# Kernel optimization log

Hardware: AMD Instinct MI355X
Metric: run time of the kernel (lower is better)

Reference implementation:

```python
import jax, jax.numpy as jnp
import numpy as np

OBS, ACT, HID, MIX, TOPK = 64, 16, 256, 16, 4
EPS = 1e-5

def _ln(x, g, b):
    m = jnp.mean(x, axis=-1, keepdims=True)
    v = jnp.mean(jnp.square(x - m), axis=-1, keepdims=True)
    return (x - m) * jax.lax.rsqrt(v + EPS) * g + b

def setup_inputs() -> dict:
    key = jax.random.key(0)
    ks = jax.random.split(key, 12)
    B = 16384
    D = OBS + ACT            # 80
    F = HID * MIX            # 4096
    s = lambda fan_in: 1.0 / np.sqrt(fan_in)
    return {
        "x": jax.random.normal(ks[0], (B, OBS), jnp.float32),
        "a": jax.random.normal(ks[1], (B, ACT), jnp.float32),
        "W1": jax.random.uniform(ks[2], (F, D), jnp.float32, -s(D), s(D)),
        "b1": jnp.zeros((F,), jnp.float32),
        "W2": jax.random.uniform(ks[3], (F, F), jnp.float32, -s(F), s(F)),
        "b2": jnp.zeros((F,), jnp.float32),
        "W3": jax.random.uniform(ks[4], (1, HID), jnp.float32, -s(HID), s(HID)),
        "b3": jnp.zeros((1,), jnp.float32),
        "g1": jnp.ones((F,), jnp.float32),
        "be1": jnp.zeros((F,), jnp.float32),
        "g2": jnp.ones((F,), jnp.float32),
        "be2": jnp.zeros((F,), jnp.float32),
        "Wg": jax.random.uniform(ks[5], (MIX, D), jnp.float32, -s(D), s(D)),
        "bg": jnp.zeros((MIX,), jnp.float32),
    }

def reference(x, a, W1, b1, W2, b2, W3, b3, g1, be1, g2, be2, Wg, bg):
    B = x.shape[0]
    xa = jnp.concatenate([x, a], axis=1)                      # [B, D]
    gate_scores = jax.nn.softmax(xa @ Wg.T + bg, axis=-1)     # [B, MIX]
    topk_vals, topk_idx = jax.lax.top_k(gate_scores, TOPK)    # [B, K]
    # renormalize top-k weights, scatter into dense score tensor
    topk_vals = topk_vals / jnp.sum(topk_vals, axis=-1, keepdims=True)
    scores = jnp.zeros_like(gate_scores).at[
        jnp.arange(B)[:, None], topk_idx].set(topk_vals)      # [B, MIX]
    h = jax.nn.relu(_ln(xa @ W1.T + b1, g1, be1))             # [B, HID*MIX]
    h = jax.nn.relu(_ln(h @ W2.T + b2, g2, be2))              # [B, HID*MIX]
    h = h.reshape(B, HID, MIX)                                # row-major, same as torch
    h = jnp.mean(h * scores[:, None, :], axis=-1)             # [B, HID]
    return h @ W3.T + b3                                      # [B, 1]
```

## Files before the change

### kernel.cpp

```cpp
#include <hip/hip_runtime.h>
#include <stdint.h>

#define OBS 64
#define ACTD 16
#define DIN 80
#define MIX 16
#define FF 4096
#define NB 16384
#define CHUNK 4096
#define KP 96
#define LNEPS 1e-5f

typedef float f32x4 __attribute__((ext_vector_type(4)));
typedef short bf16x8 __attribute__((ext_vector_type(8)));

__device__ __forceinline__ unsigned short f2bf(float f) {
    union { float f; uint32_t u; } v; v.f = f;
    uint32_t u = v.u;
    u += 0x7fff + ((u >> 16) & 1);
    return (unsigned short)(u >> 16);
}
__device__ __forceinline__ float bf2f(unsigned short h) {
    union { uint32_t u; float f; } v; v.u = ((uint32_t)h) << 16;
    return v.f;
}

__global__ __launch_bounds__(256) void k_conv(const float* __restrict__ W,
                                              unsigned short* __restrict__ O, int n4) {
    int i = blockIdx.x * 256 + threadIdx.x;
    if (i >= n4) return;
    float4 v = ((const float4*)W)[i];
    ushort4 o;
    o.x = f2bf(v.x); o.y = f2bf(v.y); o.z = f2bf(v.z); o.w = f2bf(v.w);
    ((ushort4*)O)[i] = o;
}

__global__ __launch_bounds__(256) void k_prep_x(const float* __restrict__ x, const float* __restrict__ a,
                                                unsigned short* __restrict__ xab) {
    int row = blockIdx.x * 256 + threadIdx.x;
    const float4* xp = (const float4*)(x + (size_t)row * OBS);
    unsigned short* o = xab + (size_t)row * KP;
#pragma unroll
    for (int i = 0; i < 16; ++i) {
        float4 v = xp[i];
        ushort4 u; u.x = f2bf(v.x); u.y = f2bf(v.y); u.z = f2bf(v.z); u.w = f2bf(v.w);
        ((ushort4*)o)[i] = u;
    }
    const float4* ap = (const float4*)(a + (size_t)row * ACTD);
#pragma unroll
    for (int i = 0; i < 4; ++i) {
        float4 v = ap[i];
        ushort4 u; u.x = f2bf(v.x); u.y = f2bf(v.y); u.z = f2bf(v.z); u.w = f2bf(v.w);
        ((ushort4*)(o + OBS))[i] = u;
    }
    ushort4 t0; t0.x = 0x3F80; t0.y = 0; t0.z = 0; t0.w = 0;
    ushort4 z;  z.x = 0; z.y = 0; z.z = 0; z.w = 0;
    ((ushort4*)(o + 80))[0] = t0;
    ((ushort4*)(o + 84))[0] = z;
    ((ushort4*)(o + 88))[0] = z;
    ((ushort4*)(o + 92))[0] = z;
}

__global__ __launch_bounds__(256) void k_prep_w1(const float* __restrict__ W1, const float* __restrict__ b1,
                                                 unsigned short* __restrict__ W1b) {
    int f = blockIdx.x * 256 + threadIdx.x;
    const float4* wp = (const float4*)(W1 + (size_t)f * DIN);
    unsigned short* o = W1b + (size_t)f * KP;
#pragma unroll
    for (int i = 0; i < 20; ++i) {
        float4 v = wp[i];
        ushort4 u; u.x = f2bf(v.x); u.y = f2bf(v.y); u.z = f2bf(v.z); u.w = f2bf(v.w);
        ((ushort4*)o)[i] = u;
    }
    ushort4 t0; t0.x = f2bf(b1[f]); t0.y = 0; t0.z = 0; t0.w = 0;
    ushort4 z;  z.x = 0; z.y = 0; z.z = 0; z.w = 0;
    ((ushort4*)(o + 80))[0] = t0;
    ((ushort4*)(o + 84))[0] = z;
    ((ushort4*)(o + 88))[0] = z;
    ((ushort4*)(o + 92))[0] = z;
}

__global__ __launch_bounds__(256) void k_gate(const float* __restrict__ x, const float* __restrict__ a,
                                              const float* __restrict__ Wg, const float* __restrict__ bg,
                                              float* __restrict__ scores) {
    __shared__ float wgs[MIX * DIN];
    __shared__ float bgs[MIX];
    int t = threadIdx.x;
    for (int e = t; e < MIX * DIN; e += 256) wgs[e] = Wg[e];
    if (t < MIX) bgs[t] = bg[t];
    __syncthreads();
    int row = blockIdx.x * 256 + t;
    float xa[DIN];
    const float4* xp = (const float4*)(x + (size_t)row * OBS);
#pragma unroll
    for (int i = 0; i < OBS / 4; ++i) {
        float4 v = xp[i];
        xa[i*4] = v.x; xa[i*4+1] = v.y; xa[i*4+2] = v.z; xa[i*4+3] = v.w;
    }
    const float4* ap = (const float4*)(a + (size_t)row * ACTD);
#pragma unroll
    for (int i = 0; i < ACTD / 4; ++i) {
        float4 v = ap[i];
        xa[OBS+i*4] = v.x; xa[OBS+i*4+1] = v.y; xa[OBS+i*4+2] = v.z; xa[OBS+i*4+3] = v.w;
    }
    double p[MIX];
    double mx = -1e300;
#pragma unroll
    for (int m = 0; m < MIX; ++m) {
        double acc = (double)bgs[m];
#pragma unroll
        for (int k = 0; k < DIN; ++k) acc += (double)xa[k] * (double)wgs[m*DIN + k];
        p[m] = acc;
        if (acc > mx) mx = acc;
    }
#pragma unroll
    for (int m = 0; m < MIX; ++m) p[m] = exp(p[m] - mx);
    unsigned used = 0;
    double s4 = 0.0;
#pragma unroll
    for (int j = 0; j < 4; ++j) {
        int best = 0; double bv = -1.0;
#pragma unroll
        for (int m = 0; m < MIX; ++m)
            if (!((used >> m) & 1) && p[m] > bv) { bv = p[m]; best = m; }
        used |= 1u << best;
        s4 += bv;
    }
    float* so = scores + (size_t)row * MIX;
#pragma unroll
    for (int m = 0; m < MIX; ++m)
        so[m] = ((used >> m) & 1) ? (float)(p[m] / s4) : 0.f;
}

__global__ __launch_bounds__(256) void k_gemm1(const unsigned short* __restrict__ A,
                                               const unsigned short* __restrict__ B,
                                               unsigned short* __restrict__ C,
                                               float* __restrict__ pstats) {
    __shared__ alignas(16) unsigned short As[128 * 32];
    __shared__ alignas(16) unsigned short Bs[128 * 32];
    int t = threadIdx.x;
    int pm = blockIdx.x & 31;
    int pn = blockIdx.x >> 5;
    int lane = t & 63, wid = t >> 6, wm = wid >> 1, wn = wid & 1;

    const unsigned short* Ap = A + (size_t)pm * 128 * KP;
    const unsigned short* Bp = B + (size_t)pn * 128 * KP;

    f32x4 acc[4][4] = {};

    for (int k0 = 0; k0 < KP; k0 += 32) {
#pragma unroll
        for (int i = 0; i < 2; ++i) {
            int u = t + i * 256;
            int row = u >> 2, p = u & 3;
            int ls = p ^ ((row >> 1) & 3);
            __builtin_amdgcn_global_load_lds(
                (const __attribute__((address_space(1))) void*)(Ap + (size_t)row * KP + k0 + ls * 8),
                (__attribute__((address_space(3))) void*)(As + u * 8), 16, 0, 0);
            __builtin_amdgcn_global_load_lds(
                (const __attribute__((address_space(1))) void*)(Bp + (size_t)row * KP + k0 + ls * 8),
                (__attribute__((address_space(3))) void*)(Bs + u * 8), 16, 0, 0);
        }
        __syncthreads();
        bf16x8 af[4], bfr[4];
#pragma unroll
        for (int mf = 0; mf < 4; ++mf) {
            int r = wm * 64 + mf * 16 + (lane & 15);
            int p = (lane >> 4) ^ ((r >> 1) & 3);
            af[mf] = *(const bf16x8*)(As + r * 32 + p * 8);
        }
#pragma unroll
        for (int nf = 0; nf < 4; ++nf) {
            int r = wn * 64 + nf * 16 + (lane & 15);
            int p = (lane >> 4) ^ ((r >> 1) & 3);
            bfr[nf] = *(const bf16x8*)(Bs + r * 32 + p * 8);
        }
#pragma unroll
        for (int mf = 0; mf < 4; ++mf)
#pragma unroll
            for (int nf = 0; nf < 4; ++nf)
                acc[mf][nf] = __builtin_amdgcn_mfma_f32_16x16x32_bf16(af[mf], bfr[nf], acc[mf][nf], 0, 0, 0);
        __syncthreads();
    }

    int rowbase = pm * 128 + wm * 64 + (lane >> 4) * 4;
    int colbase = pn * 128 + wn * 64 + (lane & 15);
#pragma unroll
    for (int mf = 0; mf < 4; ++mf) {
#pragma unroll
        for (int rr = 0; rr < 4; ++rr) {
            float ss = 0.f, qq = 0.f;
#pragma unroll
            for (int nf = 0; nf < 4; ++nf) {
                float v = acc[mf][nf][rr];
                ss += v; qq += v * v;
                C[(size_t)(rowbase + mf * 16 + rr) * FF + colbase + nf * 16] = f2bf(v);
            }
#pragma unroll
            for (int mask = 1; mask <= 8; mask <<= 1) {
                ss += __shfl_xor(ss, mask);
                qq += __shfl_xor(qq, mask);
            }
            if ((lane & 15) == 0) {
                int row = rowbase + mf * 16 + rr;
                int j = pn * 2 + wn;
                pstats[((size_t)row * 64 + j) * 2 + 0] = ss;
                pstats[((size_t)row * 64 + j) * 2 + 1] = qq;
            }
        }
    }
}

__global__ __launch_bounds__(256) void k_ln1(unsigned short* __restrict__ h1,
                                             const float* __restrict__ pstats,
                                             const float* __restrict__ g1, const float* __restrict__ be1) {
    __shared__ float st[8][2];
    int t = threadIdx.x;
    int r0 = blockIdx.x * 8;
    if (t < 8) {
        float s = 0.f, q = 0.f;
        const float* pp = pstats + (size_t)(r0 + t) * 128;
#pragma unroll
        for (int j = 0; j < 64; ++j) { s += pp[j * 2]; q += pp[j * 2 + 1]; }
        float mu = s / (float)FF;
        float var = q / (float)FF - mu * mu;
        st[t][0] = mu;
        st[t][1] = rsqrtf(var + LNEPS);
    }
    __syncthreads();
    int c = t * 16;
    float g[16], b[16];
#pragma unroll
    for (int q = 0; q < 4; ++q) {
        float4 gv = *(const float4*)(g1 + c + q * 4);
        float4 bv = *(const float4*)(be1 + c + q * 4);
        g[q*4] = gv.x; g[q*4+1] = gv.y; g[q*4+2] = gv.z; g[q*4+3] = gv.w;
        b[q*4] = bv.x; b[q*4+1] = bv.y; b[q*4+2] = bv.z; b[q*4+3] = bv.w;
    }
    for (int r = 0; r < 8; ++r) {
        float mu = st[r][0], rs = st[r][1];
        unsigned short* hp = h1 + (size_t)(r0 + r) * FF + c;
        uint4 u0 = *(const uint4*)hp;
        uint4 u1 = *(const uint4*)(hp + 8);
        uint32_t uu[8] = {u0.x, u0.y, u0.z, u0.w, u1.x, u1.y, u1.z, u1.w};
        uint32_t oo[8];
#pragma unroll
        for (int q = 0; q < 8; ++q) {
            float v0 = bf2f((unsigned short)(uu[q] & 0xffff));
            float v1 = bf2f((unsigned short)(uu[q] >> 16));
            float o0 = fmaxf((v0 - mu) * rs * g[q*2]   + b[q*2],   0.f);
            float o1 = fmaxf((v1 - mu) * rs * g[q*2+1] + b[q*2+1], 0.f);
            oo[q] = (uint32_t)f2bf(o0) | ((uint32_t)f2bf(o1) << 16);
        }
        uint4 w0; w0.x = oo[0]; w0.y = oo[1]; w0.z = oo[2]; w0.w = oo[3];
        uint4 w1; w1.x = oo[4]; w1.y = oo[5]; w1.z = oo[6]; w1.w = oo[7];
        *(uint4*)hp = w0;
        *(uint4*)(hp + 8) = w1;
    }
}

__global__ __launch_bounds__(512, 1) void k_gemm2(const unsigned short* __restrict__ A,
                                                  const unsigned short* __restrict__ B,
                                                  unsigned short* __restrict__ C) {
    constexpr int K = FF;
    constexpr int NKT = K / 64;
    __shared__ alignas(16) unsigned short As[2][2][8192];
    __shared__ alignas(16) unsigned short Bs[2][2][8192];

    int t = threadIdx.x;
    int lane = t & 63, wid = t >> 6;
    int wm = wid >> 2, wn = wid & 3;

    int bid = blockIdx.x;
    int xcd = bid & 7, w = bid >> 3;
    int pm = (xcd >> 1) * 4 + (w >> 3);
    int pn = (xcd & 1) * 8 + (w & 7);

    const unsigned short* Ap = A + (size_t)pm * 256 * K;
    const unsigned short* Bp = B + (size_t)pn * 256 * K;

    f32x4 acc[8][4] = {};
    bf16x8 af[4][2], bfr[4][2];

#define STAGE_H(bq, kt, H)                                                                 \
    {                                                                                      \
        const unsigned short* gsrc = ((H) < 2) ? Ap : Bp;                                  \
        unsigned short* ldst = ((H) < 2) ? &As[(bq)][(H) & 1][0] : &Bs[(bq)][(H) & 1][0];  \
        _Pragma("unroll")                                                                  \
        for (int i = 0; i < 2; ++i) {                                                      \
            int u = i * 512 + t;                                                           \
            int r = u >> 3, sl = u & 7;                                                    \
            __builtin_amdgcn_global_load_lds(                                              \
                (const __attribute__((address_space(1))) void*)(gsrc +                     \
                    (size_t)(((H) & 1) * 128 + r) * K + (kt) * 64 + ((sl ^ (r & 7)) * 8)), \
                (__attribute__((address_space(3))) void*)(ldst + u * 8), 16, 0, 0);        \
        }                                                                                  \
    }

#define RD_AF(bq, mh)                                                           \
    _Pragma("unroll") for (int m = 0; m < 4; ++m) {                             \
        int rr = (mh) * 64 + m * 16 + (lane & 15);                              \
        _Pragma("unroll") for (int kk = 0; kk < 2; ++kk) {                      \
            int sl = (kk * 4 + (lane >> 4)) ^ (rr & 7);                         \
            af[m][kk] = *(const bf16x8*)(&As[(bq)][wm][0] + rr * 64 + sl * 8);  \
        }                                                                       \
    }

#define RD_BF(bq, np)                                                           \
    _Pragma("unroll") for (int n = 0; n < 2; ++n) {                             \
        int cc = wn * 64 + ((np) * 2 + n) * 16 + (lane & 15);                   \
        int hb = cc >> 7, rr = cc & 127;                                        \
        _Pragma("unroll") for (int kk = 0; kk < 2; ++kk) {                      \
            int sl = (kk * 4 + (lane >> 4)) ^ (rr & 7);                         \
            bfr[(np) * 2 + n][kk] = *(const bf16x8*)(&Bs[(bq)][hb][0] + rr * 64 + sl * 8); \
        }                                                                       \
    }

#define MFMA_Q(mh, np)                                                          \
    __builtin_amdgcn_s_barrier();                                               \
    asm volatile("s_waitcnt lgkmcnt(0)" ::: "memory");                          \
    __builtin_amdgcn_sched_barrier(0);                                          \
    __builtin_amdgcn_s_setprio(1);                                              \
    _Pragma("unroll") for (int kk = 0; kk < 2; ++kk)                            \
    _Pragma("unroll") for (int m = 0; m < 4; ++m)                               \
    _Pragma("unroll") for (int n = 0; n < 2; ++n)                               \
        acc[(mh) * 4 + m][(np) * 2 + n] = __builtin_amdgcn_mfma_f32_16x16x32_bf16( \
            af[m][kk], bfr[(np) * 2 + n][kk], acc[(mh) * 4 + m][(np) * 2 + n], 0, 0, 0); \
    __builtin_amdgcn_s_setprio(0);                                              \
    __builtin_amdgcn_sched_barrier(0);

    STAGE_H(0, 0, 0); STAGE_H(0, 0, 1); STAGE_H(0, 0, 2); STAGE_H(0, 0, 3);
    STAGE_H(1, 1, 2); STAGE_H(1, 1, 3);
    asm volatile("s_waitcnt vmcnt(4)" ::: "memory");
    __builtin_amdgcn_s_barrier();

    for (int i = 0; i < NKT / 2; ++i) {
        int tA = 2 * i + 1;
        int tB = 2 * i + 2; if (tB > NKT - 1) tB = NKT - 1;
        int tC = 2 * i + 3; if (tC > NKT - 1) tC = NKT - 1;

        RD_AF(0, 0); RD_BF(0, 0);
        STAGE_H(1, tA, 0);
        MFMA_Q(0, 0);
        __builtin_amdgcn_s_barrier();
        RD_BF(0, 1);
        STAGE_H(1, tA, 1);
        MFMA_Q(0, 1);
        __builtin_amdgcn_s_barrier();
        RD_AF(0, 1);
        STAGE_H(0, tB, 2);
        MFMA_Q(1, 0);
        __builtin_amdgcn_s_barrier();
        STAGE_H(0, tB, 3);
        MFMA_Q(1, 1);
        asm volatile("s_waitcnt vmcnt(4)" ::: "memory");
        __builtin_amdgcn_s_barrier();

        RD_AF(1, 0); RD_BF(1, 0);
        STAGE_H(0, tB, 0);
        MFMA_Q(0, 0);
        __builtin_amdgcn_s_barrier();
        RD_BF(1, 1);
        STAGE_H(0, tB, 1);
        MFMA_Q(0, 1);
        __builtin_amdgcn_s_barrier();
        RD_AF(1, 1);
        STAGE_H(1, tC, 2);
        MFMA_Q(1, 0);
        __builtin_amdgcn_s_barrier();
        STAGE_H(1, tC, 3);
        MFMA_Q(1, 1);
        asm volatile("s_waitcnt vmcnt(4)" ::: "memory");
        __builtin_amdgcn_s_barrier();
    }
#undef STAGE_H
#undef RD_AF
#undef RD_BF
#undef MFMA_Q

    int row0 = pm * 256 + wm * 128 + (lane >> 4) * 4;
    int col0 = pn * 256 + wn * 64 + (lane & 15);
#pragma unroll
    for (int gm = 0; gm < 8; ++gm)
#pragma unroll
        for (int gn = 0; gn < 4; ++gn)
#pragma unroll
            for (int rr = 0; rr < 4; ++rr)
                C[(size_t)(row0 + gm * 16 + rr) * FF + col0 + gn * 16] = f2bf(acc[gm][gn][rr]);
}

__global__ __launch_bounds__(256) void k_epi(const unsigned short* __restrict__ y2,
                                             const float* __restrict__ scores,
                                             const float* __restrict__ b2,
                                             const float* __restrict__ g2, const float* __restrict__ be2,
                                             const float* __restrict__ W3, const float* __restrict__ b3,
                                             float* __restrict__ out) {
    int row = blockIdx.x, t = threadIdx.x;
    int lane = t & 63, wid = t >> 6;
    __shared__ float sS[MIX];
    __shared__ float rA[4], rB[4];
    __shared__ float stats[2];
    const unsigned short* yp = y2 + (size_t)row * FF + t * 16;
    uint4 u0 = *(const uint4*)yp;
    uint4 u1 = *(const uint4*)(yp + 8);
    float v[16];
    v[0]  = bf2f((unsigned short)(u0.x & 0xffff)); v[1]  = bf2f((unsigned short)(u0.x >> 16));
    v[2]  = bf2f((unsigned short)(u0.y & 0xffff)); v[3]  = bf2f((unsigned short)(u0.y >> 16));
    v[4]  = bf2f((unsigned short)(u0.z & 0xffff)); v[5]  = bf2f((unsigned short)(u0.z >> 16));
    v[6]  = bf2f((unsigned short)(u0.w & 0xffff)); v[7]  = bf2f((unsigned short)(u0.w >> 16));
    v[8]  = bf2f((unsigned short)(u1.x & 0xffff)); v[9]  = bf2f((unsigned short)(u1.x >> 16));
    v[10] = bf2f((unsigned short)(u1.y & 0xffff)); v[11] = bf2f((unsigned short)(u1.y >> 16));
    v[12] = bf2f((unsigned short)(u1.z & 0xffff)); v[13] = bf2f((unsigned short)(u1.z >> 16));
    v[14] = bf2f((unsigned short)(u1.w & 0xffff)); v[15] = bf2f((unsigned short)(u1.w >> 16));
    const float* b2p = b2 + t * 16;
#pragma unroll
    for (int blk = 0; blk < 4; ++blk) {
        float4 q = *(const float4*)(b2p + blk * 4);
        v[blk*4+0] += q.x; v[blk*4+1] += q.y; v[blk*4+2] += q.z; v[blk*4+3] += q.w;
    }
    if (t < MIX) sS[t] = scores[(size_t)row * MIX + t];
    float s = 0.f, sq = 0.f;
#pragma unroll
    for (int j = 0; j < 16; ++j) { s += v[j]; sq += v[j] * v[j]; }
#pragma unroll
    for (int off = 32; off >= 1; off >>= 1) {
        s  += __shfl_down(s, off);
        sq += __shfl_down(sq, off);
    }
    if (lane == 0) { rA[wid] = s; rB[wid] = sq; }
    __syncthreads();
    if (t == 0) {
        float S = rA[0] + rA[1] + rA[2] + rA[3];
        float Q = rB[0] + rB[1] + rB[2] + rB[3];
        float mu = S / (float)FF;
        float var = Q / (float)FF - mu * mu;
        stats[0] = mu;
        stats[1] = rsqrtf(var + LNEPS);
    }
    __syncthreads();
    float mu = stats[0], rs = stats[1];
    const float* gp = g2 + t * 16;
    const float* bp = be2 + t * 16;
    float accum = 0.f;
#pragma unroll
    for (int blk = 0; blk < 4; ++blk) {
        float4 gg = *(const float4*)(gp + blk * 4);
        float4 bb = *(const float4*)(bp + blk * 4);
        float ga[4] = {gg.x, gg.y, gg.z, gg.w};
        float ba[4] = {bb.x, bb.y, bb.z, bb.w};
#pragma unroll
        for (int jj = 0; jj < 4; ++jj) {
            int m = blk * 4 + jj;
            float o = (v[m] - mu) * rs * ga[jj] + ba[jj];
            o = fmaxf(o, 0.f);
            accum += o * sS[m];
        }
    }
    float part = accum * W3[t] * 0.0625f;
#pragma unroll
    for (int off = 32; off >= 1; off >>= 1) part += __shfl_down(part, off);
    if (lane == 0) rA[wid] = part;
    __syncthreads();
    if (t == 0) out[row] = rA[0] + rA[1] + rA[2] + rA[3] + b3[0];
}

extern "C" void kernel_launch(void* const* d_in, const int* in_sizes, int n_in,
                              void* d_out, int out_size, void* d_ws, size_t ws_size,
                              hipStream_t stream) {
    const float* x   = (const float*)d_in[0];
    const float* a   = (const float*)d_in[1];
    const float* W1  = (const float*)d_in[2];
    const float* b1  = (const float*)d_in[3];
    const float* W2  = (const float*)d_in[4];
    const float* b2  = (const float*)d_in[5];
    const float* W3  = (const float*)d_in[6];
    const float* b3  = (const float*)d_in[7];
    const float* g1  = (const float*)d_in[8];
    const float* be1 = (const float*)d_in[9];
    const float* g2  = (const float*)d_in[10];
    const float* be2 = (const float*)d_in[11];
    const float* Wg  = (const float*)d_in[12];
    const float* bg  = (const float*)d_in[13];
    float* out = (float*)d_out;

    char* ws = (char*)d_ws;
    unsigned short* W2b    = (unsigned short*)ws;
    float*          scores = (float*)(ws + 33554432ull);
    unsigned short* h1c    = (unsigned short*)(ws + 34603008ull);
    unsigned short* y2c    = (unsigned short*)(ws + 68157440ull);
    unsigned short* xabc   = (unsigned short*)(ws + 68157440ull);
    unsigned short* W1b    = (unsigned short*)(ws + 68157440ull + 786432ull);
    float*          pstats = (float*)(ws + 68157440ull + 1572864ull);

    k_conv<<<(FF * FF / 4 + 255) / 256, 256, 0, stream>>>(W2, W2b, FF * FF / 4);
    k_gate<<<NB / 256, 256, 0, stream>>>(x, a, Wg, bg, scores);

    for (int c = 0; c < NB / CHUNK; ++c) {
        const float* xc = x + (size_t)c * CHUNK * OBS;
        const float* ac = a + (size_t)c * CHUNK * ACTD;
        const float* sc = scores + (size_t)c * CHUNK * MIX;
        float* oc = out + (size_t)c * CHUNK;
        k_prep_x<<<CHUNK / 256, 256, 0, stream>>>(xc, ac, xabc);
        k_prep_w1<<<FF / 256, 256, 0, stream>>>(W1, b1, W1b);
        k_gemm1<<<(CHUNK / 128) * (FF / 128), 256, 0, stream>>>(xabc, W1b, h1c, pstats);
        k_ln1<<<CHUNK / 8, 256, 0, stream>>>(h1c, pstats, g1, be1);
        k_gemm2<<<(CHUNK / 256) * (FF / 256), 512, 0, stream>>>(h1c, W2b, y2c);
        k_epi<<<CHUNK, 256, 0, stream>>>(y2c, sc, b2, g2, be2, W3, b3, oc);
    }
}
```

Measured before the change: 836.1 us.

## Restructure GEMM main loop with precomputed LDS pointers and fewer barriers

Rewrites the bf16 MFMA GEMM K-loop so each K-tile uses one wait-plus-barrier at the start and one barrier at the end, instead of a barrier before every MFMA quarter. The next tile's global-to-LDS loads are interleaved between MFMA groups. Swizzled global and LDS addresses are precomputed once as per-thread pointers and advanced by a constant each tile, which cuts per-iteration address arithmetic. The aim is to reduce synchronization stalls and integer overhead while keeping double-buffered prefetch. The price is less fine-grained overlap guarantees and reliance on careful vmcnt accounting.

Result: faster. 742.6 us (-11.2%).

```diff
diff --git a/kernel.cpp b/kernel.cpp
--- a/kernel.cpp
+++ b/kernel.cpp
@@ -279,104 +279,104 @@
     const unsigned short* Ap = A + (size_t)pm * 256 * K;
     const unsigned short* Bp = B + (size_t)pn * 256 * K;
 
+    int l15 = lane & 15, l4 = lane >> 4;
+    int slk0 = (l4 ^ (l15 & 7)) * 16;
+    int slk1 = ((4 + l4) ^ (l15 & 7)) * 16;
+    const char* Abase = (const char*)&As[0][0][0];
+    const char* Bbase = (const char*)&Bs[0][0][0];
+    const char* afp0 = Abase + wm * 16384 + l15 * 128 + slk0;
+    const char* afp1 = Abase + wm * 16384 + l15 * 128 + slk1;
+    const char* bfp0 = Bbase + (wn >> 1) * 16384 + (wn & 1) * 8192 + l15 * 128 + slk0;
+    const char* bfp1 = Bbase + (wn >> 1) * 16384 + (wn & 1) * 8192 + l15 * 128 + slk1;
+
+    int r0 = t >> 3;
+    int swz = ((t & 7) ^ (r0 & 7)) * 8;
+    const unsigned short* sA0 = Ap + (size_t)(r0)       * K + swz;
+    const unsigned short* sA1 = Ap + (size_t)(64 + r0)  * K + swz;
+    const unsigned short* sA2 = Ap + (size_t)(128 + r0) * K + swz;
+    const unsigned short* sA3 = Ap + (size_t)(192 + r0) * K + swz;
+    const unsigned short* sB0 = Bp + (size_t)(r0)       * K + swz;
+    const unsigned short* sB1 = Bp + (size_t)(64 + r0)  * K + swz;
+    const unsigned short* sB2 = Bp + (size_t)(128 + r0) * K + swz;
+    const unsigned short* sB3 = Bp + (size_t)(192 + r0) * K + swz;
+    char* dA = (char*)&As[0][0][0] + t * 16;
+    char* dB = (char*)&Bs[0][0][0] + t * 16;
+
     f32x4 acc[8][4] = {};
     bf16x8 af[4][2], bfr[4][2];
 
-#define STAGE_H(bq, kt, H)                                                                 \
-    {                                                                                      \
-        const unsigned short* gsrc = ((H) < 2) ? Ap : Bp;                                  \
-        unsigned short* ldst = ((H) < 2) ? &As[(bq)][(H) & 1][0] : &Bs[(bq)][(H) & 1][0];  \
-        _Pragma("unroll")                                                                  \
-        for (int i = 0; i < 2; ++i) {                                                      \
-            int u = i * 512 + t;                                                           \
-            int r = u >> 3, sl = u & 7;                                                    \
-            __builtin_amdgcn_global_load_lds(                                              \
-                (const __attribute__((address_space(1))) void*)(gsrc +                     \
-                    (size_t)(((H) & 1) * 128 + r) * K + (kt) * 64 + ((sl ^ (r & 7)) * 8)), \
-                (__attribute__((address_space(3))) void*)(ldst + u * 8), 16, 0, 0);        \
-        }                                                                                  \
-    }
-
-#define RD_AF(bq, mh)                                                           \
-    _Pragma("unroll") for (int m = 0; m < 4; ++m) {                             \
-        int rr = (mh) * 64 + m * 16 + (lane & 15);                              \
-        _Pragma("unroll") for (int kk = 0; kk < 2; ++kk) {                      \
-            int sl = (kk * 4 + (lane >> 4)) ^ (rr & 7);                         \
-            af[m][kk] = *(const bf16x8*)(&As[(bq)][wm][0] + rr * 64 + sl * 8);  \
-        }                                                                       \
-    }
-
-#define RD_BF(bq, np)                                                           \
-    _Pragma("unroll") for (int n = 0; n < 2; ++n) {                             \
-        int cc = wn * 64 + ((np) * 2 + n) * 16 + (lane & 15);                   \
-        int hb = cc >> 7, rr = cc & 127;                                        \
-        _Pragma("unroll") for (int kk = 0; kk < 2; ++kk) {                      \
-            int sl = (kk * 4 + (lane >> 4)) ^ (rr & 7);                         \
-            bfr[(np) * 2 + n][kk] = *(const bf16x8*)(&Bs[(bq)][hb][0] + rr * 64 + sl * 8); \
-        }                                                                       \
-    }
-
-#define MFMA_Q(mh, np)                                                          \
-    __builtin_amdgcn_s_barrier();                                               \
-    asm volatile("s_waitcnt lgkmcnt(0)" ::: "memory");                          \
-    __builtin_amdgcn_sched_barrier(0);                                          \
-    __builtin_amdgcn_s_setprio(1);                                              \
-    _Pragma("unroll") for (int kk = 0; kk < 2; ++kk)                            \
-    _Pragma("unroll") for (int m = 0; m < 4; ++m)                               \
-    _Pragma("unroll") for (int n = 0; n < 2; ++n)                               \
-        acc[(mh) * 4 + m][(np) * 2 + n] = __builtin_amdgcn_mfma_f32_16x16x32_bf16( \
-            af[m][kk], bfr[(np) * 2 + n][kk], acc[(mh) * 4 + m][(np) * 2 + n], 0, 0, 0); \
-    __builtin_amdgcn_s_setprio(0);                                              \
+#define STG_A(BUF, HH, p0, p1)                                                              \
+    __builtin_amdgcn_global_load_lds((const __attribute__((address_space(1))) void*)(p0),   \
+        (__attribute__((address_space(3))) void*)(dA + (BUF)*32768 + (HH)*16384), 16, 0, 0);\
+    __builtin_amdgcn_global_load_lds((const __attribute__((address_space(1))) void*)(p1),   \
+        (__attribute__((address_space(3))) void*)(dA + (BUF)*32768 + (HH)*16384 + 8192), 16, 0, 0);
+#define STG_B(BUF, HH, p0, p1)                                                              \
+    __builtin_amdgcn_global_load_lds((const __attribute__((address_space(1))) void*)(p0),   \
+        (__attribute__((address_space(3))) void*)(dB + (BUF)*32768 + (HH)*16384), 16, 0, 0);\
+    __builtin_amdgcn_global_load_lds((const __attribute__((address_space(1))) void*)(p1),   \
+        (__attribute__((address_space(3))) void*)(dB + (BUF)*32768 + (HH)*16384 + 8192), 16, 0, 0);
+
+#define RD_AF(BUF, MH)                                                                      \
+    _Pragma("unroll") for (int m = 0; m < 4; ++m) {                                         \
+        af[m][0] = *(const bf16x8*)(afp0 + (BUF)*32768 + (MH)*8192 + m*2048);               \
+        af[m][1] = *(const bf16x8*)(afp1 + (BUF)*32768 + (MH)*8192 + m*2048);               \
+    }
+#define RD_BF(BUF)                                                                          \
+    _Pragma("unroll") for (int n2 = 0; n2 < 4; ++n2) {                                      \
+        bfr[n2][0] = *(const bf16x8*)(bfp0 + (BUF)*32768 + n2*2048);                        \
+        bfr[n2][1] = *(const bf16x8*)(bfp1 + (BUF)*32768 + n2*2048);                        \
+    }
+
+#define MFMA_Q(MB, NLO)                                                                     \
+    __builtin_amdgcn_s_setprio(1);                                                          \
+    _Pragma("unroll") for (int kk = 0; kk < 2; ++kk)                                        \
+    _Pragma("unroll") for (int m = 0; m < 4; ++m)                                           \
+    _Pragma("unroll") for (int n = (NLO); n < (NLO) + 2; ++n)                               \
+        acc[(MB)*4 + m][n] = __builtin_amdgcn_mfma_f32_16x16x32_bf16(                       \
+            af[m][kk], bfr[n][kk], acc[(MB)*4 + m][n], 0, 0, 0);                            \
+    __builtin_amdgcn_s_setprio(0);                                                          \
     __builtin_amdgcn_sched_barrier(0);
 
-    STAGE_H(0, 0, 0); STAGE_H(0, 0, 1); STAGE_H(0, 0, 2); STAGE_H(0, 0, 3);
-    STAGE_H(1, 1, 2); STAGE_H(1, 1, 3);
-    asm volatile("s_waitcnt vmcnt(4)" ::: "memory");
-    __builtin_amdgcn_s_barrier();
-
-    for (int i = 0; i < NKT / 2; ++i) {
-        int tA = 2 * i + 1;
-        int tB = 2 * i + 2; if (tB > NKT - 1) tB = NKT - 1;
-        int tC = 2 * i + 3; if (tC > NKT - 1) tC = NKT - 1;
-
-        RD_AF(0, 0); RD_BF(0, 0);
-        STAGE_H(1, tA, 0);
-        MFMA_Q(0, 0);
-        __builtin_amdgcn_s_barrier();
-        RD_BF(0, 1);
-        STAGE_H(1, tA, 1);
-        MFMA_Q(0, 1);
-        __builtin_amdgcn_s_barrier();
-        RD_AF(0, 1);
-        STAGE_H(0, tB, 2);
-        MFMA_Q(1, 0);
-        __builtin_amdgcn_s_barrier();
-        STAGE_H(0, tB, 3);
-        MFMA_Q(1, 1);
-        asm volatile("s_waitcnt vmcnt(4)" ::: "memory");
-        __builtin_amdgcn_s_barrier();
-
-        RD_AF(1, 0); RD_BF(1, 0);
-        STAGE_H(0, tB, 0);
-        MFMA_Q(0, 0);
-        __builtin_amdgcn_s_barrier();
-        RD_BF(1, 1);
-        STAGE_H(0, tB, 1);
-        MFMA_Q(0, 1);
-        __builtin_amdgcn_s_barrier();
-        RD_AF(1, 1);
-        STAGE_H(1, tC, 2);
-        MFMA_Q(1, 0);
-        __builtin_amdgcn_s_barrier();
-        STAGE_H(1, tC, 3);
-        MFMA_Q(1, 1);
-        asm volatile("s_waitcnt vmcnt(4)" ::: "memory");
-        __builtin_amdgcn_s_barrier();
-    }
-#undef STAGE_H
+#define TILE(BUF, DO_STAGE)                                                                 \
+    if (DO_STAGE) { STG_A(1 - (BUF), 0, sA0, sA1) }                                         \
+    if (DO_STAGE) asm volatile("s_waitcnt vmcnt(2)" ::: "memory");                          \
+    else          asm volatile("s_waitcnt vmcnt(0)" ::: "memory");                          \
+    __builtin_amdgcn_s_barrier();                                                           \
+    __builtin_amdgcn_sched_barrier(0);                                                      \
+    RD_AF(BUF, 0) RD_BF(BUF)                                                                \
+    MFMA_Q(0, 0)                                                                            \
+    if (DO_STAGE) { STG_A(1 - (BUF), 1, sA2, sA3) }                                         \
+    MFMA_Q(0, 2)                                                                            \
+    if (DO_STAGE) { STG_B(1 - (BUF), 0, sB0, sB1) }                                         \
+    RD_AF(BUF, 1)                                                                           \
+    MFMA_Q(1, 0)                                                                            \
+    if (DO_STAGE) { STG_B(1 - (BUF), 1, sB2, sB3) }                                         \
+    MFMA_Q(1, 2)                                                                            \
+    asm volatile("" ::: "memory");                                                          \
+    __builtin_amdgcn_s_barrier();                                                           \
+    asm volatile("" ::: "memory");                                                          \
+    if (DO_STAGE) { sA0 += 64; sA1 += 64; sA2 += 64; sA3 += 64;                             \
+                    sB0 += 64; sB1 += 64; sB2 += 64; sB3 += 64; }
+
+    STG_A(0, 0, sA0, sA1) STG_A(0, 1, sA2, sA3)
+    STG_B(0, 0, sB0, sB1) STG_B(0, 1, sB2, sB3)
+    sA0 += 64; sA1 += 64; sA2 += 64; sA3 += 64;
+    sB0 += 64; sB1 += 64; sB2 += 64; sB3 += 64;
+    asm volatile("" ::: "memory");
+
+    for (int i = 0; i < NKT / 2 - 1; ++i) {
+        TILE(0, true)
+        TILE(1, true)
+    }
+    TILE(0, true)
+    TILE(1, false)
+
+#undef STG_A
+#undef STG_B
 #undef RD_AF
 #undef RD_BF
 #undef MFMA_Q
+#undef TILE
 
     int row0 = pm * 256 + wm * 128 + (lane >> 4) * 4;
     int col0 = pn * 256 + wn * 64 + (lane & 15);
```
